# Performance work log

Measured on AMD Instinct MI355X. Metric: run time of the kernel, lower is better.

The kernel has to match this reference:

```python
import jax, jax.numpy as jnp
import numpy as np

EPS_NORM = 1e-12
EPS_ENT = 1e-12
TEMPERATURE = 0.5
CONTRAST_DENOM = 128.0 * 100.0


def _l2_normalize(x, axis=-1):
    n = jnp.linalg.norm(x, axis=axis, keepdims=True)
    return x / jnp.maximum(n, EPS_NORM)


def setup_inputs() -> dict:
    key0 = jax.random.key(0)
    k1, k2, k3, k4 = jax.random.split(key0, 4)
    B, L, C = 16, 2048, 512
    M = 512
    return {
        "key": jax.random.normal(k1, (B, L, C), dtype=jnp.float32),
        "query": jax.random.normal(k2, (B, L, C), dtype=jnp.float32),
        "keys": jax.random.uniform(k3, (M, C), dtype=jnp.float32),
        "values": jax.random.uniform(k4, (M, C), dtype=jnp.float32),
        "mode": 0,
    }


def reference(key, query, keys, values, mode):
    B, L, C = key.shape
    k = _l2_normalize(key.reshape(-1, C))    # [T, C]
    q = _l2_normalize(query.reshape(-1, C))  # [T, C]

    # --- gatheringLoss ---
    score = jnp.einsum('tc,mc->tm', k, keys)            # [T, M]
    # top-1 of softmax(score) == argmax(score) (softmax is monotone)
    idx = jnp.argmax(score, axis=1)                     # [T]
    nearest_values = values[idx]                        # [T, C]
    gathering_loss = jnp.mean((q - nearest_values) ** 2)

    logits = score / TEMPERATURE                        # [T, M]
    logp = jax.nn.log_softmax(logits, axis=-1)
    gathered = jnp.take_along_axis(logp, idx[:, None], axis=1)  # [T, 1]
    contrast_loss = jnp.sum(gathered) / (-CONTRAST_DENOM)

    # --- read ---
    weights = jax.nn.softmax(score, axis=-1)            # [T, M]
    # EntropyLoss: mean over rows of -sum(w * log(w + eps))
    entropy_loss = jnp.mean(-jnp.sum(weights * jnp.log(weights + EPS_ENT), axis=-1))
    read_query = weights @ values                       # [T, C]

    return (read_query.reshape(B, L, C), entropy_loss, gathering_loss,
            contrast_loss, keys, values)
```

## Files before the change

kernel.cpp:

```cpp
#include <hip/hip_runtime.h>

typedef short short8 __attribute__((ext_vector_type(8)));
typedef float floatx4 __attribute__((ext_vector_type(4)));

#define C_DIM 512
#define KQ_STRIDE 1040

__device__ __forceinline__ unsigned short f2bf(float f) {
    unsigned u = __builtin_bit_cast(unsigned, f);
    u = u + 0x7fffu + ((u >> 16) & 1u);
    return (unsigned short)(u >> 16);
}

__global__ __launch_bounds__(256) void pack_kernel(
    const float* __restrict__ keys, const float* __restrict__ values,
    unsigned short* __restrict__ keysFrag, unsigned short* __restrict__ valsFrag) {
    int tid = blockIdx.x * 256 + threadIdx.x;
    int e  = tid & 32767;
    int l  = e & 63;
    int NT = (e >> 6) & 31;
    int kt = e >> 11;
    int li = l & 15, q4 = l >> 4;
    unsigned short tmp[8];
    if (tid < 32768) {
        const float* s = keys + (size_t)(NT * 16 + li) * C_DIM + kt * 32 + q4 * 8;
#pragma unroll
        for (int j = 0; j < 8; j++) tmp[j] = f2bf(s[j]);
        unsigned short* d = keysFrag + ((size_t)(kt * 32 + NT) * 64 + l) * 8;
        *(ushort4*)d       = make_ushort4(tmp[0], tmp[1], tmp[2], tmp[3]);
        *(ushort4*)(d + 4) = make_ushort4(tmp[4], tmp[5], tmp[6], tmp[7]);
    } else {
#pragma unroll
        for (int j = 0; j < 8; j++)
            tmp[j] = f2bf(values[(size_t)(kt * 32 + q4 * 8 + j) * C_DIM + NT * 16 + li]);
        unsigned short* d = valsFrag + ((size_t)(kt * 32 + NT) * 64 + l) * 8;
        *(ushort4*)d       = make_ushort4(tmp[0], tmp[1], tmp[2], tmp[3]);
        *(ushort4*)(d + 4) = make_ushort4(tmp[4], tmp[5], tmp[6], tmp[7]);
    }
}

__global__ __launch_bounds__(512, 4) void fused_kernel(
    const float* __restrict__ key,
    const float* __restrict__ query,
    const unsigned short* __restrict__ keysFrag,
    const unsigned short* __restrict__ valsFrag,
    const float* __restrict__ values,
    float* __restrict__ outRQ,
    float* __restrict__ scal) {
    __shared__ char kq[64 * KQ_STRIDE];
    __shared__ float stats[8][64][6];
    __shared__ float finals[64][2];
    __shared__ int   idxsh[64];
    __shared__ float gpart[8];

    const int tid = threadIdx.x;
    const int w  = tid >> 6;
    const int l  = tid & 63;
    const int li = l & 15;
    const int q4 = l >> 4;
    const int row0 = blockIdx.x << 6;

#pragma unroll
    for (int it = 0; it < 2; it++) {
        int r = (w << 3) + (it << 2) + q4;
        const float4* src = (const float4*)(key + (size_t)(row0 + r) * C_DIM);
        float4 v[8];
        float ss = 0.f;
#pragma unroll
        for (int i = 0; i < 8; i++) {
            v[i] = src[i * 16 + li];
            ss += v[i].x * v[i].x + v[i].y * v[i].y + v[i].z * v[i].z + v[i].w * v[i].w;
        }
#pragma unroll
        for (int m = 1; m < 16; m <<= 1) ss += __shfl_xor(ss, m, 64);
        float inv = 1.0f / fmaxf(sqrtf(ss), 1e-12f);
        char* dstrow = kq + r * KQ_STRIDE;
#pragma unroll
        for (int i = 0; i < 8; i++) {
            ushort4 b = make_ushort4(f2bf(v[i].x * inv), f2bf(v[i].y * inv),
                                     f2bf(v[i].z * inv), f2bf(v[i].w * inv));
            *(ushort4*)(dstrow + i * 128 + li * 8) = b;
        }
    }
    __syncthreads();

    floatx4 acc1[16];
#pragma unroll
    for (int i = 0; i < 16; i++) acc1[i] = (floatx4){0.f, 0.f, 0.f, 0.f};
    {
        const short8* kf = (const short8*)keysFrag;
        short8 bcur[4], bnxt[4];
#pragma unroll
        for (int nt = 0; nt < 4; nt++) bcur[nt] = kf[(size_t)((w * 4 + nt) * 64 + l)];
        for (int kt = 0; kt < 16; kt++) {
            if (kt < 15) {
#pragma unroll
                for (int nt = 0; nt < 4; nt++)
                    bnxt[nt] = kf[(size_t)(((kt + 1) * 32 + w * 4 + nt) * 64 + l)];
            }
            short8 a[4];
#pragma unroll
            for (int rg = 0; rg < 4; rg++)
                a[rg] = *(const short8*)(kq + (rg * 16 + li) * KQ_STRIDE + kt * 64 + q4 * 16);
#pragma unroll
            for (int rg = 0; rg < 4; rg++)
#pragma unroll
                for (int nt = 0; nt < 4; nt++)
                    acc1[rg * 4 + nt] = __builtin_amdgcn_mfma_f32_16x16x32_bf16(
                        a[rg], bcur[nt], acc1[rg * 4 + nt], 0, 0, 0);
#pragma unroll
            for (int nt = 0; nt < 4; nt++) bcur[nt] = bnxt[nt];
        }
    }

#pragma unroll
    for (int rg = 0; rg < 4; rg++) {
#pragma unroll
        for (int reg = 0; reg < 4; reg++) {
            float m = acc1[rg * 4][reg];
            int bi = w * 64 + li;
#pragma unroll
            for (int nt = 1; nt < 4; nt++) {
                float s = acc1[rg * 4 + nt][reg];
                if (s > m) { m = s; bi = w * 64 + nt * 16 + li; }
            }
            float z1 = 0.f, e1 = 0.f, z2 = 0.f;
#pragma unroll
            for (int nt = 0; nt < 4; nt++) {
                float s = acc1[rg * 4 + nt][reg];
                float p = __expf(s - m);
                z1 += p; e1 += p * s; z2 += p * p;
            }
#pragma unroll
            for (int msk = 1; msk < 16; msk <<= 1) {
                float mo  = __shfl_xor(m,  msk, 64);
                float z1o = __shfl_xor(z1, msk, 64);
                float e1o = __shfl_xor(e1, msk, 64);
                float z2o = __shfl_xor(z2, msk, 64);
                int   bio = __shfl_xor(bi, msk, 64);
                if (mo > m) {
                    float sc = __expf(m - mo);
                    z1 = z1 * sc + z1o; e1 = e1 * sc + e1o; z2 = z2 * sc * sc + z2o;
                    m = mo; bi = bio;
                } else if (mo == m) {
                    z1 += z1o; e1 += e1o; z2 += z2o; bi = min(bi, bio);
                } else {
                    float sc = __expf(mo - m);
                    z1 += z1o * sc; e1 += e1o * sc; z2 += z2o * sc * sc;
                }
            }
            if (li == 0) {
                float* st = stats[w][rg * 16 + q4 * 4 + reg];
                st[0] = m; st[1] = z1; st[2] = e1; st[3] = z2;
                ((int*)st)[4] = bi;
            }
        }
    }
    __syncthreads();

    if (tid < 64) {
        int r = tid;
        const float* st0 = stats[0][r];
        float m = st0[0], z1 = st0[1], e1 = st0[2], z2 = st0[3];
        int bi = ((const int*)st0)[4];
#pragma unroll
        for (int p = 1; p < 8; p++) {
            const float* st = stats[p][r];
            float mo = st[0], z1o = st[1], e1o = st[2], z2o = st[3];
            int bio = ((const int*)st)[4];
            if (mo > m) {
                float sc = __expf(m - mo);
                z1 = z1 * sc + z1o; e1 = e1 * sc + e1o; z2 = z2 * sc * sc + z2o;
                m = mo; bi = bio;
            } else if (mo == m) {
                z1 += z1o; e1 += e1o; z2 += z2o; bi = min(bi, bio);
            } else {
                float sc = __expf(mo - m);
                z1 += z1o * sc; e1 += e1o * sc; z2 += z2o * sc * sc;
            }
        }
        finals[r][0] = m;
        finals[r][1] = 1.0f / z1;
        idxsh[r] = bi;
        float ent = m + __logf(z1) - e1 / z1;
        float con = __logf(z2);
#pragma unroll
        for (int msk = 1; msk < 64; msk <<= 1) {
            ent += __shfl_xor(ent, msk, 64);
            con += __shfl_xor(con, msk, 64);
        }
        if (tid == 0) {
            atomicAdd(&scal[0], ent * (1.0f / 32768.0f));
            atomicAdd(&scal[2], con * (1.0f / 12800.0f));
        }
    }
    __syncthreads();

#pragma unroll
    for (int rg = 0; rg < 4; rg++) {
#pragma unroll
        for (int reg = 0; reg < 4; reg++) {
            int r = rg * 16 + q4 * 4 + reg;
            float m1 = finals[r][0];
#pragma unroll
            for (int nt = 0; nt < 4; nt++) {
                float p = __expf(acc1[rg * 4 + nt][reg] - m1);
                int col = w * 64 + nt * 16 + li;
                *(unsigned short*)(kq + r * KQ_STRIDE + col * 2) = f2bf(p);
            }
        }
    }
    __syncthreads();

    floatx4 acc2[16];
#pragma unroll
    for (int i = 0; i < 16; i++) acc2[i] = (floatx4){0.f, 0.f, 0.f, 0.f};
    {
        const short8* vf = (const short8*)valsFrag;
        short8 bcur[4], bnxt[4];
#pragma unroll
        for (int nt = 0; nt < 4; nt++) bcur[nt] = vf[(size_t)((w * 4 + nt) * 64 + l)];
        for (int kt = 0; kt < 16; kt++) {
            if (kt < 15) {
#pragma unroll
                for (int nt = 0; nt < 4; nt++)
                    bnxt[nt] = vf[(size_t)(((kt + 1) * 32 + w * 4 + nt) * 64 + l)];
            }
            short8 a[4];
#pragma unroll
            for (int rg = 0; rg < 4; rg++)
                a[rg] = *(const short8*)(kq + (rg * 16 + li) * KQ_STRIDE + kt * 64 + q4 * 16);
#pragma unroll
            for (int rg = 0; rg < 4; rg++)
#pragma unroll
                for (int nt = 0; nt < 4; nt++)
                    acc2[rg * 4 + nt] = __builtin_amdgcn_mfma_f32_16x16x32_bf16(
                        a[rg], bcur[nt], acc2[rg * 4 + nt], 0, 0, 0);
#pragma unroll
            for (int nt = 0; nt < 4; nt++) bcur[nt] = bnxt[nt];
        }
    }

#pragma unroll
    for (int rg = 0; rg < 4; rg++) {
#pragma unroll
        for (int reg = 0; reg < 4; reg++) {
            int r = rg * 16 + q4 * 4 + reg;
            float iz = finals[r][1];
            float* orow = outRQ + (size_t)(row0 + r) * C_DIM + w * 64 + li;
#pragma unroll
            for (int nt = 0; nt < 4; nt++) orow[nt * 16] = acc2[rg * 4 + nt][reg] * iz;
        }
    }

    float gacc = 0.f;
#pragma unroll
    for (int rr = 0; rr < 8; rr++) {
        int r = (w << 3) + rr;
        const float4* qr = (const float4*)(query + (size_t)(row0 + r) * C_DIM);
        float4 a = qr[l * 2], b = qr[l * 2 + 1];
        float ss = a.x * a.x + a.y * a.y + a.z * a.z + a.w * a.w +
                   b.x * b.x + b.y * b.y + b.z * b.z + b.w * b.w;
#pragma unroll
        for (int m = 1; m < 64; m <<= 1) ss += __shfl_xor(ss, m, 64);
        float inv = 1.0f / fmaxf(sqrtf(ss), 1e-12f);
        const float4* vr = (const float4*)(values + (size_t)idxsh[r] * C_DIM);
        float4 va = vr[l * 2], vb = vr[l * 2 + 1];
        float d;
        d = a.x * inv - va.x; gacc += d * d;
        d = a.y * inv - va.y; gacc += d * d;
        d = a.z * inv - va.z; gacc += d * d;
        d = a.w * inv - va.w; gacc += d * d;
        d = b.x * inv - vb.x; gacc += d * d;
        d = b.y * inv - vb.y; gacc += d * d;
        d = b.z * inv - vb.z; gacc += d * d;
        d = b.w * inv - vb.w; gacc += d * d;
    }
#pragma unroll
    for (int m = 1; m < 64; m <<= 1) gacc += __shfl_xor(gacc, m, 64);
    if (l == 0) gpart[w] = gacc;
    __syncthreads();
    if (tid == 0) {
        float s = 0.f;
#pragma unroll
        for (int i = 0; i < 8; i++) s += gpart[i];
        atomicAdd(&scal[1], s * (1.0f / (32768.0f * 512.0f)));
    }
}

extern "C" void kernel_launch(void* const* d_in, const int* in_sizes, int n_in,
                              void* d_out, int out_size, void* d_ws, size_t ws_size,
                              hipStream_t stream) {
    (void)in_sizes; (void)n_in; (void)out_size; (void)ws_size;
    const float* key    = (const float*)d_in[0];
    const float* query  = (const float*)d_in[1];
    const float* keysIn = (const float*)d_in[2];
    const float* valsIn = (const float*)d_in[3];
    float* out = (float*)d_out;

    unsigned short* keysFrag = (unsigned short*)d_ws;
    unsigned short* valsFrag = keysFrag + 512 * 512;

    float* outRQ   = out;
    float* scal    = out + 16777216;
    float* keysOut = out + 16777219;
    float* valsOut = keysOut + 262144;

    hipMemsetAsync(scal, 0, 3 * sizeof(float), stream);
    hipMemcpyAsync(keysOut, keysIn, 262144 * sizeof(float), hipMemcpyDeviceToDevice, stream);
    hipMemcpyAsync(valsOut, valsIn, 262144 * sizeof(float), hipMemcpyDeviceToDevice, stream);

    pack_kernel<<<256, 256, 0, stream>>>(keysIn, valsIn, keysFrag, valsFrag);
    fused_kernel<<<512, 512, 0, stream>>>(key, query, keysFrag, valsFrag, valsIn, outRQ, scal);
}
```

Baseline: 246.2 us.

## Halve rows per block, defer key normalization, fold copies into pack kernel

The fused kernel now handles 32 rows per block instead of 64, using half the accumulators and LDS, and raises the launch-bounds occupancy hint from 4 to 6 while doubling the grid. Key rows are stored in LDS unnormalized and the inverse norm is applied to the scores afterwards. The gathering loss is computed algebraically from the query norm, the dot product and precomputed value norms. The memset and the two device memcpys are folded into the pack kernel to cut launches. Halving the rows per block doubles how often each block streams the key and value fragments from global memory, and rounding the unnormalized keys to bf16 changes the numerics slightly.

```diff
diff --git a/kernel.cpp b/kernel.cpp
--- a/kernel.cpp
+++ b/kernel.cpp
@@ -14,43 +14,69 @@
 
 __global__ __launch_bounds__(256) void pack_kernel(
     const float* __restrict__ keys, const float* __restrict__ values,
-    unsigned short* __restrict__ keysFrag, unsigned short* __restrict__ valsFrag) {
-    int tid = blockIdx.x * 256 + threadIdx.x;
-    int e  = tid & 32767;
-    int l  = e & 63;
-    int NT = (e >> 6) & 31;
-    int kt = e >> 11;
-    int li = l & 15, q4 = l >> 4;
-    unsigned short tmp[8];
-    if (tid < 32768) {
-        const float* s = keys + (size_t)(NT * 16 + li) * C_DIM + kt * 32 + q4 * 8;
-#pragma unroll
-        for (int j = 0; j < 8; j++) tmp[j] = f2bf(s[j]);
-        unsigned short* d = keysFrag + ((size_t)(kt * 32 + NT) * 64 + l) * 8;
-        *(ushort4*)d       = make_ushort4(tmp[0], tmp[1], tmp[2], tmp[3]);
-        *(ushort4*)(d + 4) = make_ushort4(tmp[4], tmp[5], tmp[6], tmp[7]);
+    unsigned short* __restrict__ keysFrag, unsigned short* __restrict__ valsFrag,
+    float* __restrict__ vnorm2,
+    float* __restrict__ keysOut, float* __restrict__ valsOut,
+    float* __restrict__ scal) {
+    const int bx = blockIdx.x, tx = threadIdx.x;
+    if (bx < 256) {
+        int tid = bx * 256 + tx;
+        int e  = tid & 32767;
+        int l  = e & 63;
+        int NT = (e >> 6) & 31;
+        int kt = e >> 11;
+        int li = l & 15, q4 = l >> 4;
+        unsigned short tmp[8];
+        if (tid < 32768) {
+            const float* s = keys + (size_t)(NT * 16 + li) * C_DIM + kt * 32 + q4 * 8;
+#pragma unroll
+            for (int j = 0; j < 8; j++) tmp[j] = f2bf(s[j]);
+            unsigned short* d = keysFrag + ((size_t)(kt * 32 + NT) * 64 + l) * 8;
+            *(ushort4*)d       = make_ushort4(tmp[0], tmp[1], tmp[2], tmp[3]);
+            *(ushort4*)(d + 4) = make_ushort4(tmp[4], tmp[5], tmp[6], tmp[7]);
+        } else {
+#pragma unroll
+            for (int j = 0; j < 8; j++)
+                tmp[j] = f2bf(values[(size_t)(kt * 32 + q4 * 8 + j) * C_DIM + NT * 16 + li]);
+            unsigned short* d = valsFrag + ((size_t)(kt * 32 + NT) * 64 + l) * 8;
+            *(ushort4*)d       = make_ushort4(tmp[0], tmp[1], tmp[2], tmp[3]);
+            *(ushort4*)(d + 4) = make_ushort4(tmp[4], tmp[5], tmp[6], tmp[7]);
+        }
     } else {
-#pragma unroll
-        for (int j = 0; j < 8; j++)
-            tmp[j] = f2bf(values[(size_t)(kt * 32 + q4 * 8 + j) * C_DIM + NT * 16 + li]);
-        unsigned short* d = valsFrag + ((size_t)(kt * 32 + NT) * 64 + l) * 8;
-        *(ushort4*)d       = make_ushort4(tmp[0], tmp[1], tmp[2], tmp[3]);
-        *(ushort4*)(d + 4) = make_ushort4(tmp[4], tmp[5], tmp[6], tmp[7]);
+        int tid2 = (bx - 256) * 256 + tx;
+        int row = tid2 >> 2, seg = tid2 & 3;
+        const float4* src = (const float4*)(values + (size_t)row * C_DIM + seg * 128);
+        float ss = 0.f;
+#pragma unroll
+        for (int i = 0; i < 32; i++) {
+            float4 v = src[i];
+            ss += v.x * v.x + v.y * v.y + v.z * v.z + v.w * v.w;
+        }
+        ss += __shfl_xor(ss, 1, 64);
+        ss += __shfl_xor(ss, 2, 64);
+        if (seg == 0) vnorm2[row] = ss;
+        if (bx == 256 && tx == 0) { scal[0] = 0.f; scal[1] = 0.f; scal[2] = 0.f; }
+    }
+    int gtid = bx * 256 + tx;
+    if (gtid < 65536) {
+        ((float4*)keysOut)[gtid] = ((const float4*)keys)[gtid];
+        ((float4*)valsOut)[gtid] = ((const float4*)values)[gtid];
     }
 }
 
-__global__ __launch_bounds__(512, 4) void fused_kernel(
+__global__ __launch_bounds__(512, 6) void fused_kernel(
     const float* __restrict__ key,
     const float* __restrict__ query,
     const unsigned short* __restrict__ keysFrag,
     const unsigned short* __restrict__ valsFrag,
     const float* __restrict__ values,
+    const float* __restrict__ vnorm2,
     float* __restrict__ outRQ,
     float* __restrict__ scal) {
-    __shared__ char kq[64 * KQ_STRIDE];
-    __shared__ float stats[8][64][6];
-    __shared__ float finals[64][2];
-    __shared__ int   idxsh[64];
+    __shared__ char kq[32 * KQ_STRIDE];
+    __shared__ float stats[8][32][5];
+    __shared__ float m1s[32], invks[32], invzs[32];
+    __shared__ int   idxsh[32];
     __shared__ float gpart[8];
 
     const int tid = threadIdx.x;
@@ -58,35 +84,29 @@
     const int l  = tid & 63;
     const int li = l & 15;
     const int q4 = l >> 4;
-    const int row0 = blockIdx.x << 6;
-
-#pragma unroll
-    for (int it = 0; it < 2; it++) {
-        int r = (w << 3) + (it << 2) + q4;
+    const int row0 = blockIdx.x << 5;
+
+    {
+        int r = (w << 2) + q4;
         const float4* src = (const float4*)(key + (size_t)(row0 + r) * C_DIM);
-        float4 v[8];
+        char* dstrow = kq + r * KQ_STRIDE;
         float ss = 0.f;
 #pragma unroll
         for (int i = 0; i < 8; i++) {
-            v[i] = src[i * 16 + li];
-            ss += v[i].x * v[i].x + v[i].y * v[i].y + v[i].z * v[i].z + v[i].w * v[i].w;
+            float4 v = src[i * 16 + li];
+            *(ushort4*)(dstrow + i * 128 + li * 8) =
+                make_ushort4(f2bf(v.x), f2bf(v.y), f2bf(v.z), f2bf(v.w));
+            ss += v.x * v.x + v.y * v.y + v.z * v.z + v.w * v.w;
         }
 #pragma unroll
         for (int m = 1; m < 16; m <<= 1) ss += __shfl_xor(ss, m, 64);
-        float inv = 1.0f / fmaxf(sqrtf(ss), 1e-12f);
-        char* dstrow = kq + r * KQ_STRIDE;
-#pragma unroll
-        for (int i = 0; i < 8; i++) {
-            ushort4 b = make_ushort4(f2bf(v[i].x * inv), f2bf(v[i].y * inv),
-                                     f2bf(v[i].z * inv), f2bf(v[i].w * inv));
-            *(ushort4*)(dstrow + i * 128 + li * 8) = b;
-        }
-    }
-    __syncthreads();
-
-    floatx4 acc1[16];
-#pragma unroll
-    for (int i = 0; i < 16; i++) acc1[i] = (floatx4){0.f, 0.f, 0.f, 0.f};
+        if (li == 0) invks[r] = 1.0f / fmaxf(sqrtf(ss), 1e-12f);
+    }
+    __syncthreads();
+
+    floatx4 acc[8];
+#pragma unroll
+    for (int i = 0; i < 8; i++) acc[i] = (floatx4){0.f, 0.f, 0.f, 0.f};
     {
         const short8* kf = (const short8*)keysFrag;
         short8 bcur[4], bnxt[4];
@@ -98,38 +118,37 @@
                 for (int nt = 0; nt < 4; nt++)
                     bnxt[nt] = kf[(size_t)(((kt + 1) * 32 + w * 4 + nt) * 64 + l)];
             }
-            short8 a[4];
-#pragma unroll
-            for (int rg = 0; rg < 4; rg++)
-                a[rg] = *(const short8*)(kq + (rg * 16 + li) * KQ_STRIDE + kt * 64 + q4 * 16);
-#pragma unroll
-            for (int rg = 0; rg < 4; rg++)
-#pragma unroll
-                for (int nt = 0; nt < 4; nt++)
-                    acc1[rg * 4 + nt] = __builtin_amdgcn_mfma_f32_16x16x32_bf16(
-                        a[rg], bcur[nt], acc1[rg * 4 + nt], 0, 0, 0);
+            short8 a0 = *(const short8*)(kq + li * KQ_STRIDE + kt * 64 + q4 * 16);
+            short8 a1 = *(const short8*)(kq + (16 + li) * KQ_STRIDE + kt * 64 + q4 * 16);
+#pragma unroll
+            for (int nt = 0; nt < 4; nt++) {
+                acc[nt]     = __builtin_amdgcn_mfma_f32_16x16x32_bf16(a0, bcur[nt], acc[nt], 0, 0, 0);
+                acc[4 + nt] = __builtin_amdgcn_mfma_f32_16x16x32_bf16(a1, bcur[nt], acc[4 + nt], 0, 0, 0);
+            }
 #pragma unroll
             for (int nt = 0; nt < 4; nt++) bcur[nt] = bnxt[nt];
         }
     }
 
 #pragma unroll
-    for (int rg = 0; rg < 4; rg++) {
+    for (int rg = 0; rg < 2; rg++) {
 #pragma unroll
         for (int reg = 0; reg < 4; reg++) {
-            float m = acc1[rg * 4][reg];
+            int rrow = rg * 16 + q4 * 4 + reg;
+            float invk = invks[rrow];
+            float s[4];
+#pragma unroll
+            for (int nt = 0; nt < 4; nt++) s[nt] = acc[rg * 4 + nt][reg] * invk;
+            float m = s[0];
             int bi = w * 64 + li;
 #pragma unroll
-            for (int nt = 1; nt < 4; nt++) {
-                float s = acc1[rg * 4 + nt][reg];
-                if (s > m) { m = s; bi = w * 64 + nt * 16 + li; }
-            }
+            for (int nt = 1; nt < 4; nt++)
+                if (s[nt] > m) { m = s[nt]; bi = w * 64 + nt * 16 + li; }
             float z1 = 0.f, e1 = 0.f, z2 = 0.f;
 #pragma unroll
             for (int nt = 0; nt < 4; nt++) {
-                float s = acc1[rg * 4 + nt][reg];
-                float p = __expf(s - m);
-                z1 += p; e1 += p * s; z2 += p * p;
+                float p = __expf(s[nt] - m);
+                z1 += p; e1 += p * s[nt]; z2 += p * p;
             }
 #pragma unroll
             for (int msk = 1; msk < 16; msk <<= 1) {
@@ -150,7 +169,7 @@
                 }
             }
             if (li == 0) {
-                float* st = stats[w][rg * 16 + q4 * 4 + reg];
+                float* st = stats[w][rrow];
                 st[0] = m; st[1] = z1; st[2] = e1; st[3] = z2;
                 ((int*)st)[4] = bi;
             }
@@ -158,7 +177,7 @@
     }
     __syncthreads();
 
-    if (tid < 64) {
+    if (tid < 32) {
         int r = tid;
         const float* st0 = stats[0][r];
         float m = st0[0], z1 = st0[1], e1 = st0[2], z2 = st0[3];
@@ -179,13 +198,13 @@
                 z1 += z1o * sc; e1 += e1o * sc; z2 += z2o * sc * sc;
             }
         }
-        finals[r][0] = m;
-        finals[r][1] = 1.0f / z1;
+        m1s[r] = m;
+        invzs[r] = 1.0f / z1;
         idxsh[r] = bi;
         float ent = m + __logf(z1) - e1 / z1;
         float con = __logf(z2);
 #pragma unroll
-        for (int msk = 1; msk < 64; msk <<= 1) {
+        for (int msk = 1; msk < 32; msk <<= 1) {
             ent += __shfl_xor(ent, msk, 64);
             con += __shfl_xor(con, msk, 64);
         }
@@ -197,24 +216,24 @@
     __syncthreads();
 
 #pragma unroll
-    for (int rg = 0; rg < 4; rg++) {
+    for (int rg = 0; rg < 2; rg++) {
 #pragma unroll
         for (int reg = 0; reg < 4; reg++) {
-            int r = rg * 16 + q4 * 4 + reg;
-            float m1 = finals[r][0];
+            int rrow = rg * 16 + q4 * 4 + reg;
+            float m1 = m1s[rrow];
+            float invk = invks[rrow];
 #pragma unroll
             for (int nt = 0; nt < 4; nt++) {
-                float p = __expf(acc1[rg * 4 + nt][reg] - m1);
+                float p = __expf(acc[rg * 4 + nt][reg] * invk - m1);
                 int col = w * 64 + nt * 16 + li;
-                *(unsigned short*)(kq + r * KQ_STRIDE + col * 2) = f2bf(p);
-            }
-        }
-    }
-    __syncthreads();
-
-    floatx4 acc2[16];
-#pragma unroll
-    for (int i = 0; i < 16; i++) acc2[i] = (floatx4){0.f, 0.f, 0.f, 0.f};
+                *(unsigned short*)(kq + rrow * KQ_STRIDE + col * 2) = f2bf(p);
+            }
+        }
+    }
+    __syncthreads();
+
+#pragma unroll
+    for (int i = 0; i < 8; i++) acc[i] = (floatx4){0.f, 0.f, 0.f, 0.f};
     {
         const short8* vf = (const short8*)valsFrag;
         short8 bcur[4], bnxt[4];
@@ -226,59 +245,54 @@
                 for (int nt = 0; nt < 4; nt++)
                     bnxt[nt] = vf[(size_t)(((kt + 1) * 32 + w * 4 + nt) * 64 + l)];
             }
-            short8 a[4];
-#pragma unroll
-            for (int rg = 0; rg < 4; rg++)
-                a[rg] = *(const short8*)(kq + (rg * 16 + li) * KQ_STRIDE + kt * 64 + q4 * 16);
-#pragma unroll
-            for (int rg = 0; rg < 4; rg++)
-#pragma unroll
-                for (int nt = 0; nt < 4; nt++)
-                    acc2[rg * 4 + nt] = __builtin_amdgcn_mfma_f32_16x16x32_bf16(
-                        a[rg], bcur[nt], acc2[rg * 4 + nt], 0, 0, 0);
+            short8 a0 = *(const short8*)(kq + li * KQ_STRIDE + kt * 64 + q4 * 16);
+            short8 a1 = *(const short8*)(kq + (16 + li) * KQ_STRIDE + kt * 64 + q4 * 16);
+#pragma unroll
+            for (int nt = 0; nt < 4; nt++) {
+                acc[nt]     = __builtin_amdgcn_mfma_f32_16x16x32_bf16(a0, bcur[nt], acc[nt], 0, 0, 0);
+                acc[4 + nt] = __builtin_amdgcn_mfma_f32_16x16x32_bf16(a1, bcur[nt], acc[4 + nt], 0, 0, 0);
+            }
 #pragma unroll
             for (int nt = 0; nt < 4; nt++) bcur[nt] = bnxt[nt];
         }
     }
 
 #pragma unroll
-    for (int rg = 0; rg < 4; rg++) {
+    for (int rg = 0; rg < 2; rg++) {
 #pragma unroll
         for (int reg = 0; reg < 4; reg++) {
-            int r = rg * 16 + q4 * 4 + reg;
-            float iz = finals[r][1];
-            float* orow = outRQ + (size_t)(row0 + r) * C_DIM + w * 64 + li;
-#pragma unroll
-            for (int nt = 0; nt < 4; nt++) orow[nt * 16] = acc2[rg * 4 + nt][reg] * iz;
-        }
-    }
-
-    float gacc = 0.f;
-#pragma unroll
-    for (int rr = 0; rr < 8; rr++) {
-        int r = (w << 3) + rr;
+            int rrow = rg * 16 + q4 * 4 + reg;
+            float iz = invzs[rrow];
+            float* orow = outRQ + (size_t)(row0 + rrow) * C_DIM + w * 64 + li;
+#pragma unroll
+            for (int nt = 0; nt < 4; nt++) orow[nt * 16] = acc[rg * 4 + nt][reg] * iz;
+        }
+    }
+
+    {
+        int r = (w << 2) + q4;
+        int mi = idxsh[r];
         const float4* qr = (const float4*)(query + (size_t)(row0 + r) * C_DIM);
-        float4 a = qr[l * 2], b = qr[l * 2 + 1];
-        float ss = a.x * a.x + a.y * a.y + a.z * a.z + a.w * a.w +
-                   b.x * b.x + b.y * b.y + b.z * b.z + b.w * b.w;
-#pragma unroll
-        for (int m = 1; m < 64; m <<= 1) ss += __shfl_xor(ss, m, 64);
-        float inv = 1.0f / fmaxf(sqrtf(ss), 1e-12f);
-        const float4* vr = (const float4*)(values + (size_t)idxsh[r] * C_DIM);
-        float4 va = vr[l * 2], vb = vr[l * 2 + 1];
-        float d;
-        d = a.x * inv - va.x; gacc += d * d;
-        d = a.y * inv - va.y; gacc += d * d;
-        d = a.z * inv - va.z; gacc += d * d;
-        d = a.w * inv - va.w; gacc += d * d;
-        d = b.x * inv - vb.x; gacc += d * d;
-        d = b.y * inv - vb.y; gacc += d * d;
-        d = b.z * inv - vb.z; gacc += d * d;
-        d = b.w * inv - vb.w; gacc += d * d;
-    }
-#pragma unroll
-    for (int m = 1; m < 64; m <<= 1) gacc += __shfl_xor(gacc, m, 64);
-    if (l == 0) gpart[w] = gacc;
+        const float4* vr = (const float4*)(values + (size_t)mi * C_DIM);
+        float ssq = 0.f, dqv = 0.f;
+#pragma unroll
+        for (int i = 0; i < 8; i++) {
+            float4 a = qr[i * 16 + li];
+            float4 b = vr[i * 16 + li];
+            ssq += a.x * a.x + a.y * a.y + a.z * a.z + a.w * a.w;
+            dqv += a.x * b.x + a.y * b.y + a.z * b.z + a.w * b.w;
+        }
+#pragma unroll
+        for (int m = 1; m < 16; m <<= 1) {
+            ssq += __shfl_xor(ssq, m, 64);
+            dqv += __shfl_xor(dqv, m, 64);
+        }
+        float g = 1.0f + vnorm2[mi] - 2.0f * dqv / fmaxf(sqrtf(ssq), 1e-12f);
+        float gl = (li == 0) ? g : 0.f;
+        gl += __shfl_xor(gl, 16, 64);
+        gl += __shfl_xor(gl, 32, 64);
+        if (l == 0) gpart[w] = gl;
+    }
     __syncthreads();
     if (tid == 0) {
         float s = 0.f;
@@ -300,16 +314,15 @@
 
     unsigned short* keysFrag = (unsigned short*)d_ws;
     unsigned short* valsFrag = keysFrag + 512 * 512;
+    float* vnorm2 = (float*)(valsFrag + 512 * 512);
 
     float* outRQ   = out;
     float* scal    = out + 16777216;
     float* keysOut = out + 16777219;
     float* valsOut = keysOut + 262144;
 
-    hipMemsetAsync(scal, 0, 3 * sizeof(float), stream);
-    hipMemcpyAsync(keysOut, keysIn, 262144 * sizeof(float), hipMemcpyDeviceToDevice, stream);
-    hipMemcpyAsync(valsOut, valsIn, 262144 * sizeof(float), hipMemcpyDeviceToDevice, stream);
-
-    pack_kernel<<<256, 256, 0, stream>>>(keysIn, valsIn, keysFrag, valsFrag);
-    fused_kernel<<<512, 512, 0, stream>>>(key, query, keysFrag, valsFrag, valsIn, outRQ, scal);
+    pack_kernel<<<264, 256, 0, stream>>>(keysIn, valsIn, keysFrag, valsFrag,
+                                         vnorm2, keysOut, valsOut, scal);
+    fused_kernel<<<1024, 512, 0, stream>>>(key, query, keysFrag, valsFrag,
+                                           valsIn, vnorm2, outRQ, scal);
 }
```

Measured after the change: 292.9 us. 1.19x slower.
